# Kernel tuning notes

Measured on AMD Instinct MI355X. Metric: run time of the kernel, lower is better.

The kernel has to match this reference:

```python
import jax, jax.numpy as jnp
import numpy as np

B, L, D, H = 4, 1024, 768, 12
DH = D // H  # 64


def setup_inputs() -> dict:
    key = jax.random.key(0)
    kx, kk, kq, kv = jax.random.split(key, 4)
    # Original uses torch.rand (uniform [0,1)); scale by 1/D so pre-softmax
    # logits stay in a numerically sane range (same math, better conditioning).
    scale = 1.0 / D
    x = jax.random.normal(kx, (B, L, D), dtype=jnp.float32)
    k = jax.random.uniform(kk, (H, D, D), dtype=jnp.float32) * scale
    q = jax.random.uniform(kq, (H, D, D), dtype=jnp.float32) * scale
    v = jax.random.uniform(kv, (H, DH, D), dtype=jnp.float32) * scale
    return {"x": x, "k": k, "q": q, "v": v}


def reference(x, k, q, v):
    # x: [B, L, D]; torch permutes to [B, D, L] then 'bdl,ncd->bncl';
    # equivalent directly: 'bld,ncd->bncl'.
    K = jnp.einsum('bld,ncd->bncl', x, k)   # [B, H, D, L]
    Q = jnp.einsum('bld,ncd->bncl', x, q)   # [B, H, D, L]
    V = jnp.einsum('bld,ncd->bncl', x, v)   # [B, H, DH, L]
    scores = jnp.einsum('bndl,bndm->bnlm', Q, K)        # [B, H, L, L]
    S = jax.nn.softmax(scores, axis=-1)                  # softmax over dim 3
    R = jnp.einsum('bnkl,bndl->bndk', S, V)              # [B, H, DH, L]
    R = R.reshape(x.shape[0], D, -1)                     # [B, D, L]
    return jnp.transpose(R, (0, 2, 1))                   # [B, L, D]
```

## Files before the change

kernel.cpp:

```cpp
#include <hip/hip_runtime.h>
#include <hip/hip_bf16.h>
#include <stdint.h>
#include <stddef.h>

typedef unsigned short u16;
typedef __attribute__((ext_vector_type(8))) short short8;
typedef __attribute__((ext_vector_type(4))) float f32x4;

#define NB 4
#define NL 1024
#define ND 768
#define NH 12
#define NDH 64

__device__ __forceinline__ u16 f2bf(float f) {
  __hip_bfloat16 h = __float2bfloat16(f);
  return *reinterpret_cast<u16*>(&h);
}
__device__ __forceinline__ float bf2f(u16 u) {
  __hip_bfloat16 h;
  *reinterpret_cast<u16*>(&h) = u;
  return __bfloat162float(h);
}

__device__ __forceinline__ void load16_to_lds(const u16* g, u16* l) {
  __builtin_amdgcn_global_load_lds(
      (__attribute__((address_space(1))) void*)(uintptr_t)g,
      (__attribute__((address_space(3))) void*)(uint32_t)(uintptr_t)l,
      16, 0, 0);
}

__global__ __launch_bounds__(256) void cast_bf16_kernel(const float* __restrict__ in,
                                                        u16* __restrict__ out, int n4) {
  int i = blockIdx.x * 256 + threadIdx.x;
  int stride = gridDim.x * 256;
  for (; i < n4; i += stride) {
    float4 f = ((const float4*)in)[i];
    ushort4 o;
    o.x = f2bf(f.x); o.y = f2bf(f.y); o.z = f2bf(f.z); o.w = f2bf(f.w);
    ((ushort4*)out)[i] = o;
  }
}

__global__ __launch_bounds__(256) void transpose_cast_kernel(const float* __restrict__ in,
                                                             u16* __restrict__ out) {
  __shared__ float tile[32][33];
  int h = blockIdx.z;
  const float* src = in + (size_t)h * ND * ND;
  u16* dst = out + (size_t)h * ND * ND;
  int c0 = blockIdx.x * 32, r0 = blockIdx.y * 32;
  int tx = threadIdx.x & 31, ty = threadIdx.x >> 5;
#pragma unroll
  for (int i = 0; i < 32; i += 8)
    tile[ty + i][tx] = src[(size_t)(r0 + ty + i) * ND + c0 + tx];
  __syncthreads();
#pragma unroll
  for (int i = 0; i < 32; i += 8)
    dst[(size_t)(c0 + ty + i) * ND + r0 + tx] = f2bf(tile[tx][ty + i]);
}

template <bool BF16_OUT, int IT, int JT, int KDIM, int LDC, int BK>
__global__ __launch_bounds__(256) void gemm_bt(
    const u16* __restrict__ A, const u16* __restrict__ Bm, void* __restrict__ Cv,
    long sAb, long sAn, long sAz,
    long sBb, long sBn, long sBz,
    long sCb, long sCn, long sCz,
    int p0) {
  constexpr int MTILE = IT * 32;
  constexpr int NTILE = JT * 32;
  constexpr int CPR = BK / 8;
  constexpr int ACH = MTILE * CPR / 256;
  constexpr int BCH = NTILE * CPR / 256;
  constexpr int KC = BK / 32;
  __shared__ __align__(16) u16 As[MTILE * BK];
  __shared__ __align__(16) u16 Bs[NTILE * BK];

  int id = blockIdx.x + gridDim.x * (blockIdx.y + gridDim.y * blockIdx.z);
  int total = gridDim.x * gridDim.y * gridDim.z;
  int xx, yy, zz;
  if ((total & 7) == 0) {
    int per = total >> 3;
    int wk = (id & 7) * per + (id >> 3);
    xx = wk % gridDim.x;
    int g2 = wk / gridDim.x;
    yy = g2 % gridDim.y;
    zz = g2 / gridDim.y;
  } else {
    xx = blockIdx.x; yy = blockIdx.y; zz = blockIdx.z;
  }

  int g = p0 + zz;
  int b = g / NH, n = g % NH;
  A  += (size_t)b * sAb + (size_t)n * sAn + (size_t)zz * sAz;
  Bm += (size_t)b * sBb + (size_t)n * sBn + (size_t)zz * sBz;
  size_t cOff = (size_t)b * sCb + (size_t)n * sCn + (size_t)zz * sCz;

  int m0 = yy * MTILE, n0 = xx * NTILE;
  int t = threadIdx.x;
  int lane = t & 63, w = t >> 6;
  int row16 = lane & 15, q = lane >> 4;
  int wm = w >> 1, wn = w & 1;
  int rsw = (BK == 32) ? ((row16 >> 1) & 3) : (row16 & 7);

  const u16* gA[ACH];
  const u16* gB[BCH];
#pragma unroll
  for (int u = 0; u < ACH; u++) {
    int c = u * 256 + t;
    int r = c / CPR;
    int sw = (BK == 32) ? ((r >> 1) & 3) : (r & 7);
    int cc = (c & (CPR - 1)) ^ sw;
    gA[u] = A + (size_t)(m0 + r) * KDIM + cc * 8;
  }
#pragma unroll
  for (int u = 0; u < BCH; u++) {
    int c = u * 256 + t;
    int r = c / CPR;
    int sw = (BK == 32) ? ((r >> 1) & 3) : (r & 7);
    int cc = (c & (CPR - 1)) ^ sw;
    gB[u] = Bm + (size_t)(n0 + r) * KDIM + cc * 8;
  }

  f32x4 acc[IT][JT];
#pragma unroll
  for (int i = 0; i < IT; i++)
#pragma unroll
    for (int j = 0; j < JT; j++) acc[i][j] = (f32x4){0.f, 0.f, 0.f, 0.f};

#pragma unroll 1
  for (int k0 = 0; k0 < KDIM; k0 += BK) {
    __syncthreads();
#pragma unroll
    for (int u = 0; u < ACH; u++) {
      load16_to_lds(gA[u], &As[(size_t)(u * 256 + w * 64) * 8]);
      gA[u] += BK;
    }
#pragma unroll
    for (int u = 0; u < BCH; u++) {
      load16_to_lds(gB[u], &Bs[(size_t)(u * 256 + w * 64) * 8]);
      gB[u] += BK;
    }
    __syncthreads();

#pragma unroll
    for (int kc = 0; kc < KC; kc++) {
      int ch = ((kc * 4 + q) ^ rsw) * 8;
      short8 af[IT], bfr[JT];
#pragma unroll
      for (int i = 0; i < IT; i++)
        af[i] = *(const short8*)&As[(wm * (IT * 16) + i * 16 + row16) * BK + ch];
#pragma unroll
      for (int j = 0; j < JT; j++)
        bfr[j] = *(const short8*)&Bs[(wn * (JT * 16) + j * 16 + row16) * BK + ch];
#pragma unroll
      for (int i = 0; i < IT; i++)
#pragma unroll
        for (int j = 0; j < JT; j++)
          acc[i][j] = __builtin_amdgcn_mfma_f32_16x16x32_bf16(af[i], bfr[j], acc[i][j], 0, 0, 0);
    }
  }

#pragma unroll
  for (int i = 0; i < IT; i++) {
    int row = m0 + wm * (IT * 16) + i * 16 + q * 4;
#pragma unroll
    for (int j = 0; j < JT; j++) {
      int col = n0 + wn * (JT * 16) + j * 16 + row16;
#pragma unroll
      for (int r = 0; r < 4; r++) {
        float vv = acc[i][j][r];
        if (BF16_OUT) {
          ((u16*)Cv)[cOff + (size_t)(row + r) * LDC + col] = f2bf(vv);
        } else {
          ((float*)Cv)[cOff + (size_t)(row + r) * LDC + col] = vv;
        }
      }
    }
  }
}

__global__ __launch_bounds__(256) void softmax_pv_kernel(
    const u16* __restrict__ Sb, const u16* __restrict__ V2, float* __restrict__ out,
    int p0) {
  __shared__ __align__(16) u16 Ps[128 * 128];
  __shared__ __align__(16) u16 Vs[64 * 128];

  int id = blockIdx.x + gridDim.x * blockIdx.y;
  int total = gridDim.x * gridDim.y;
  int xx, zz;
  if ((total & 7) == 0) {
    int per = total >> 3;
    int wk = (id & 7) * per + (id >> 3);
    xx = wk & 7; zz = wk >> 3;
  } else {
    xx = blockIdx.x; zz = blockIdx.y;
  }

  int g = p0 + zz;
  int b = g / NH, n = g % NH;
  const u16* S = Sb + (size_t)zz * NL * NL;
  const u16* V = V2 + (size_t)zz * NDH * NL;

  int l0 = xx * 128;
  int t = threadIdx.x;
  int lane = t & 63, w = t >> 6;
  int row16 = lane & 15, q = lane >> 4;
  int rs = row16 & 7;

  f32x4 acc[2][5];
#pragma unroll
  for (int i = 0; i < 2; i++)
#pragma unroll
    for (int j = 0; j < 5; j++) acc[i][j] = (f32x4){0.f, 0.f, 0.f, 0.f};

  short8 onesf;
  {
    short val = (row16 == 0) ? (short)0x3F80 : (short)0;
#pragma unroll
    for (int e = 0; e < 8; e++) onesf[e] = val;
  }

#pragma unroll 1
  for (int mt = 0; mt < 8; mt++) {
    int mo = mt * 128;
    __syncthreads();
#pragma unroll
    for (int u = 0; u < 8; u++) {
      int c = u * 256 + t;
      int r = c >> 4, cc = (c & 15) ^ (r & 7);
      load16_to_lds(S + (size_t)(l0 + r) * NL + mo + cc * 8,
                    &Ps[(size_t)(u * 256 + w * 64) * 8]);
    }
#pragma unroll
    for (int u = 0; u < 4; u++) {
      int c = u * 256 + t;
      int r = c >> 4, cc = (c & 15) ^ (r & 7);
      load16_to_lds(V + (size_t)r * NL + mo + cc * 8,
                    &Vs[(size_t)(u * 256 + w * 64) * 8]);
    }
    __syncthreads();

#pragma unroll
    for (int kk = 0; kk < 4; kk++) {
      int ch = ((kk * 4 + q) ^ rs) * 16;
      short8 af[2], bfr[4];
#pragma unroll
      for (int i = 0; i < 2; i++) {
        int row = w * 32 + i * 16 + row16;
        short8 raw = *(const short8*)((const char*)Ps + row * 256 + ch);
        short8 pe;
#pragma unroll
        for (int e = 0; e < 8; e++) pe[e] = (short)f2bf(__expf(bf2f((u16)raw[e])));
        af[i] = pe;
      }
#pragma unroll
      for (int j = 0; j < 4; j++) {
        int row = j * 16 + row16;
        bfr[j] = *(const short8*)((const char*)Vs + row * 256 + ch);
      }
#pragma unroll
      for (int i = 0; i < 2; i++) {
#pragma unroll
        for (int j = 0; j < 4; j++)
          acc[i][j] = __builtin_amdgcn_mfma_f32_16x16x32_bf16(af[i], bfr[j], acc[i][j], 0, 0, 0);
        acc[i][4] = __builtin_amdgcn_mfma_f32_16x16x32_bf16(af[i], onesf, acc[i][4], 0, 0, 0);
      }
    }
  }

#pragma unroll
  for (int i = 0; i < 2; i++) {
#pragma unroll
    for (int r = 0; r < 4; r++) {
      float sum = __shfl(acc[i][4][r], lane & 48, 64);
      float inv = 1.0f / sum;
      int row = l0 + w * 32 + i * 16 + q * 4 + r;
      float* op = out + ((size_t)b * NL + row) * ND + n * NDH;
#pragma unroll
      for (int j = 0; j < 4; j++)
        op[j * 16 + row16] = acc[i][j][r] * inv;
    }
  }
}

extern "C" void kernel_launch(void* const* d_in, const int* in_sizes, int n_in,
                              void* d_out, int out_size, void* d_ws, size_t ws_size,
                              hipStream_t stream) {
  (void)in_sizes; (void)n_in; (void)out_size;
  const float* x  = (const float*)d_in[0];
  const float* kI = (const float*)d_in[1];
  const float* qI = (const float*)d_in[2];
  const float* vI = (const float*)d_in[3];
  float* out = (float*)d_out;

  size_t off = 0;
  char* wsb = (char*)d_ws;
  auto alloc = [&](size_t bytes) -> char* {
    char* p = wsb + off;
    off += (bytes + 255) & ~(size_t)255;
    return p;
  };
  u16* xb = (u16*)alloc((size_t)NB * NL * ND * 2);
  u16* qT = (u16*)alloc((size_t)NH * ND * ND * 2);
  u16* kT = (u16*)alloc((size_t)NH * ND * ND * 2);
  u16* vb = (u16*)alloc((size_t)NH * NDH * ND * 2);
  u16* MT = (u16*)alloc((size_t)NH * ND * ND * 2);
  size_t fixedSz = off;
  const size_t perPair = (size_t)NL * ND * 2 + (size_t)NL * NL * 2 + (size_t)NDH * NL * 2;
  int chunk = NB * NH;
  if (fixedSz + (size_t)chunk * perPair > ws_size) {
    size_t avail = ws_size > fixedSz ? ws_size - fixedSz : 0;
    chunk = (int)(avail / perPair);
    if (chunk < 1) chunk = 1;
    if (chunk > NB * NH) chunk = NB * NH;
  }
  u16* T  = (u16*)alloc((size_t)chunk * NL * ND * 2);
  u16* Sb = (u16*)alloc((size_t)chunk * NL * NL * 2);
  u16* V2 = (u16*)alloc((size_t)chunk * NDH * NL * 2);

  const long DD  = (long)ND * ND;
  const long LD  = (long)NL * ND;
  const long LL  = (long)NL * NL;
  const long DHD = (long)NDH * ND;
  const long DHL = (long)NDH * NL;

  {
    int n4 = NB * NL * ND / 4;
    cast_bf16_kernel<<<dim3((n4 + 255) / 256), dim3(256), 0, stream>>>(x, xb, n4);
    int n4v = NH * NDH * ND / 4;
    cast_bf16_kernel<<<dim3((n4v + 255) / 256), dim3(256), 0, stream>>>(vI, vb, n4v);
  }
  transpose_cast_kernel<<<dim3(24, 24, NH), dim3(256), 0, stream>>>(qI, qT);
  transpose_cast_kernel<<<dim3(24, 24, NH), dim3(256), 0, stream>>>(kI, kT);

  gemm_bt<true, 4, 4, 768, ND, 64><<<dim3(6, 6, NH), dim3(256), 0, stream>>>(
      kT, qT, MT,
      0, DD, 0,  0, DD, 0,  0, DD, 0, 0);

  for (int p0 = 0; p0 < NB * NH; p0 += chunk) {
    int c = NB * NH - p0;
    if (c > chunk) c = chunk;
    gemm_bt<true, 2, 2, 768, NL, 64><<<dim3(16, 1, c), dim3(256), 0, stream>>>(
        vb, xb, V2,
        0, DHD, 0,  LD, 0, 0,  0, 0, DHL, p0);
    gemm_bt<true, 4, 4, 768, ND, 64><<<dim3(6, 8, c), dim3(256), 0, stream>>>(
        xb, MT, T,
        LD, 0, 0,  0, DD, 0,  0, 0, LD, p0);
    gemm_bt<true, 4, 4, 768, NL, 64><<<dim3(8, 8, c), dim3(256), 0, stream>>>(
        T, xb, Sb,
        0, 0, LD,  LD, 0, 0,  0, 0, LL, p0);
    softmax_pv_kernel<<<dim3(8, c), dim3(256), 0, stream>>>(Sb, V2, out, p0);
  }
}
```

Before: 348.7 us.

## Fuse score GEMM into softmax-PV kernel, keeping T tile resident in LDS

Replaces the separate T·xbᵀ score GEMM plus softmax_pv kernel with one fused kernel. Each block holds a 64-row slice of T (64x768 bf16) in LDS, computes 64x128 score tiles against streamed x tiles, exponentiates them into LDS and accumulates P·V together with row sums. This removes the write and re-read of the B*H*L*L bf16 score buffer and one launch. In exchange it uses 144KB of dynamic LDS per block (one block per CU), syncs twice per K step, and runs with fewer blocks (16 per pair) and no multi-stage pipelining.

```diff
diff --git a/kernel.cpp b/kernel.cpp
--- a/kernel.cpp
+++ b/kernel.cpp
@@ -29,6 +29,10 @@
       (__attribute__((address_space(3))) void*)(uint32_t)(uintptr_t)l,
       16, 0, 0);
 }
+
+__device__ __forceinline__ int swz8(int c, int r) { return (c ^ r) & 7; }
+__device__ __forceinline__ int swz16(int c, int r) { return (c & 8) | ((c ^ r) & 7); }
+__device__ __forceinline__ int swzT(int c, int r) { return (c & ~7) | ((c ^ r) & 7); }
 
 __global__ __launch_bounds__(256) void cast_bf16_kernel(const float* __restrict__ in,
                                                         u16* __restrict__ out, int n4) {
@@ -179,39 +183,58 @@
   }
 }
 
-__global__ __launch_bounds__(256) void softmax_pv_kernel(
-    const u16* __restrict__ Sb, const u16* __restrict__ V2, float* __restrict__ out,
-    int p0) {
-  __shared__ __align__(16) u16 Ps[128 * 128];
-  __shared__ __align__(16) u16 Vs[64 * 128];
+__global__ __launch_bounds__(256) void attn_pv_kernel(
+    const u16* __restrict__ T, const u16* __restrict__ xb, const u16* __restrict__ V2,
+    float* __restrict__ out, int p0) {
+  extern __shared__ u16 smem[];
+  u16* Ts = smem;
+  u16* Bs = smem + 49152;
+  u16* Vs = smem + 57344;
+  u16* Ss = smem + 65536;
 
   int id = blockIdx.x + gridDim.x * blockIdx.y;
-  int total = gridDim.x * gridDim.y;
-  int xx, zz;
-  if ((total & 7) == 0) {
-    int per = total >> 3;
-    int wk = (id & 7) * per + (id >> 3);
-    xx = wk & 7; zz = wk >> 3;
-  } else {
-    xx = blockIdx.x; zz = blockIdx.y;
-  }
+  int per = (gridDim.x * gridDim.y) >> 3;
+  int wk = (id & 7) * per + (id >> 3);
+  int xx = wk & 15, zz = wk >> 4;
 
   int g = p0 + zz;
   int b = g / NH, n = g % NH;
-  const u16* S = Sb + (size_t)zz * NL * NL;
-  const u16* V = V2 + (size_t)zz * NDH * NL;
-
-  int l0 = xx * 128;
+  const u16* Tz = T + (size_t)zz * NL * ND + (size_t)xx * 64 * ND;
+  const u16* xbb = xb + (size_t)b * NL * ND;
+  const u16* Vz = V2 + (size_t)zz * NDH * NL;
+  int l0 = xx * 64;
+
   int t = threadIdx.x;
   int lane = t & 63, w = t >> 6;
   int row16 = lane & 15, q = lane >> 4;
-  int rs = row16 & 7;
-
-  f32x4 acc[2][5];
-#pragma unroll
-  for (int i = 0; i < 2; i++)
-#pragma unroll
-    for (int j = 0; j < 5; j++) acc[i][j] = (f32x4){0.f, 0.f, 0.f, 0.f};
+  int wm = w >> 1, wn = w & 1;
+
+#pragma unroll
+  for (int u = 0; u < 24; u++) {
+    int c = u * 256 + t;
+    int r = c / 96, rem = c - r * 96;
+    int lg = swzT(rem, r);
+    load16_to_lds(Tz + (size_t)r * ND + lg * 8, &Ts[(size_t)(u * 256 + w * 64) * 8]);
+  }
+
+  const u16* bsrc[4];
+#pragma unroll
+  for (int u = 0; u < 4; u++) {
+    int c = u * 256 + t;
+    int r = c >> 3, cc = (c & 7) ^ (r & 7);
+    bsrc[u] = xbb + (size_t)r * ND + cc * 8;
+  }
+  const u16* vsrc[4];
+#pragma unroll
+  for (int u = 0; u < 4; u++) {
+    int c = u * 256 + t;
+    int r = c >> 4, cc = (c & 15) ^ (r & 7);
+    vsrc[u] = Vz + (size_t)r * NL + cc * 8;
+  }
+
+  f32x4 acc_o[5];
+#pragma unroll
+  for (int j = 0; j < 5; j++) acc_o[j] = (f32x4){0.f, 0.f, 0.f, 0.f};
 
   short8 onesf;
   {
@@ -225,61 +248,85 @@
     int mo = mt * 128;
     __syncthreads();
 #pragma unroll
-    for (int u = 0; u < 8; u++) {
-      int c = u * 256 + t;
-      int r = c >> 4, cc = (c & 15) ^ (r & 7);
-      load16_to_lds(S + (size_t)(l0 + r) * NL + mo + cc * 8,
-                    &Ps[(size_t)(u * 256 + w * 64) * 8]);
-    }
-#pragma unroll
-    for (int u = 0; u < 4; u++) {
-      int c = u * 256 + t;
-      int r = c >> 4, cc = (c & 15) ^ (r & 7);
-      load16_to_lds(V + (size_t)r * NL + mo + cc * 8,
-                    &Vs[(size_t)(u * 256 + w * 64) * 8]);
+    for (int u = 0; u < 4; u++)
+      load16_to_lds(vsrc[u] + mo, &Vs[(size_t)(u * 256 + w * 64) * 8]);
+
+    f32x4 acc_s[2][4];
+#pragma unroll
+    for (int i = 0; i < 2; i++)
+#pragma unroll
+      for (int j = 0; j < 4; j++) acc_s[i][j] = (f32x4){0.f, 0.f, 0.f, 0.f};
+
+#pragma unroll 1
+    for (int kb = 0; kb < 12; kb++) {
+      __syncthreads();
+#pragma unroll
+      for (int u = 0; u < 4; u++)
+        load16_to_lds(bsrc[u] + ((size_t)mo * ND + kb * 64), &Bs[(size_t)(u * 256 + w * 64) * 8]);
+      __syncthreads();
+
+#pragma unroll
+      for (int kc = 0; kc < 2; kc++) {
+        short8 af[2], bfr[4];
+#pragma unroll
+        for (int i = 0; i < 2; i++) {
+          int l = wm * 32 + i * 16 + row16;
+          int ck = kb * 8 + kc * 4 + q;
+          af[i] = *(const short8*)&Ts[l * ND + swzT(ck, l) * 8];
+        }
+#pragma unroll
+        for (int j = 0; j < 4; j++) {
+          int r = wn * 64 + j * 16 + row16;
+          bfr[j] = *(const short8*)&Bs[r * 64 + swz8(kc * 4 + q, r) * 8];
+        }
+#pragma unroll
+        for (int i = 0; i < 2; i++)
+#pragma unroll
+          for (int j = 0; j < 4; j++)
+            acc_s[i][j] = __builtin_amdgcn_mfma_f32_16x16x32_bf16(af[i], bfr[j], acc_s[i][j], 0, 0, 0);
+      }
+    }
+
+#pragma unroll
+    for (int i = 0; i < 2; i++) {
+#pragma unroll
+      for (int j = 0; j < 4; j++) {
+#pragma unroll
+        for (int r = 0; r < 4; r++) {
+          int l = wm * 32 + i * 16 + q * 4 + r;
+          int col = wn * 64 + j * 16 + row16;
+          Ss[l * 128 + swz16(col >> 3, l) * 8 + (col & 7)] = f2bf(__expf(acc_s[i][j][r]));
+        }
+      }
     }
     __syncthreads();
 
 #pragma unroll
     for (int kk = 0; kk < 4; kk++) {
-      int ch = ((kk * 4 + q) ^ rs) * 16;
-      short8 af[2], bfr[4];
-#pragma unroll
-      for (int i = 0; i < 2; i++) {
-        int row = w * 32 + i * 16 + row16;
-        short8 raw = *(const short8*)((const char*)Ps + row * 256 + ch);
-        short8 pe;
-#pragma unroll
-        for (int e = 0; e < 8; e++) pe[e] = (short)f2bf(__expf(bf2f((u16)raw[e])));
-        af[i] = pe;
+      int l = w * 16 + row16;
+      short8 af = *(const short8*)&Ss[l * 128 + swz16(kk * 4 + q, l) * 8];
+      short8 bfr[4];
+#pragma unroll
+      for (int j = 0; j < 4; j++) {
+        int dh = j * 16 + row16;
+        bfr[j] = *(const short8*)&Vs[dh * 128 + swz16(kk * 4 + q, dh) * 8];
       }
 #pragma unroll
-      for (int j = 0; j < 4; j++) {
-        int row = j * 16 + row16;
-        bfr[j] = *(const short8*)((const char*)Vs + row * 256 + ch);
-      }
-#pragma unroll
-      for (int i = 0; i < 2; i++) {
-#pragma unroll
-        for (int j = 0; j < 4; j++)
-          acc[i][j] = __builtin_amdgcn_mfma_f32_16x16x32_bf16(af[i], bfr[j], acc[i][j], 0, 0, 0);
-        acc[i][4] = __builtin_amdgcn_mfma_f32_16x16x32_bf16(af[i], onesf, acc[i][4], 0, 0, 0);
-      }
-    }
-  }
-
-#pragma unroll
-  for (int i = 0; i < 2; i++) {
-#pragma unroll
-    for (int r = 0; r < 4; r++) {
-      float sum = __shfl(acc[i][4][r], lane & 48, 64);
-      float inv = 1.0f / sum;
-      int row = l0 + w * 32 + i * 16 + q * 4 + r;
-      float* op = out + ((size_t)b * NL + row) * ND + n * NDH;
-#pragma unroll
       for (int j = 0; j < 4; j++)
-        op[j * 16 + row16] = acc[i][j][r] * inv;
-    }
+        acc_o[j] = __builtin_amdgcn_mfma_f32_16x16x32_bf16(af, bfr[j], acc_o[j], 0, 0, 0);
+      acc_o[4] = __builtin_amdgcn_mfma_f32_16x16x32_bf16(af, onesf, acc_o[4], 0, 0, 0);
+    }
+  }
+
+#pragma unroll
+  for (int r = 0; r < 4; r++) {
+    float sum = __shfl(acc_o[4][r], lane & 48, 64);
+    float inv = 1.0f / sum;
+    int row = l0 + w * 16 + q * 4 + r;
+    float* op = out + ((size_t)b * NL + row) * ND + n * NDH;
+#pragma unroll
+    for (int j = 0; j < 4; j++)
+      op[j * 16 + row16] = acc_o[j][r] * inv;
   }
 }
 
@@ -306,7 +353,7 @@
   u16* vb = (u16*)alloc((size_t)NH * NDH * ND * 2);
   u16* MT = (u16*)alloc((size_t)NH * ND * ND * 2);
   size_t fixedSz = off;
-  const size_t perPair = (size_t)NL * ND * 2 + (size_t)NL * NL * 2 + (size_t)NDH * NL * 2;
+  const size_t perPair = (size_t)NL * ND * 2 + (size_t)NDH * NL * 2;
   int chunk = NB * NH;
   if (fixedSz + (size_t)chunk * perPair > ws_size) {
     size_t avail = ws_size > fixedSz ? ws_size - fixedSz : 0;
@@ -315,14 +362,15 @@
     if (chunk > NB * NH) chunk = NB * NH;
   }
   u16* T  = (u16*)alloc((size_t)chunk * NL * ND * 2);
-  u16* Sb = (u16*)alloc((size_t)chunk * NL * NL * 2);
   u16* V2 = (u16*)alloc((size_t)chunk * NDH * NL * 2);
 
   const long DD  = (long)ND * ND;
   const long LD  = (long)NL * ND;
-  const long LL  = (long)NL * NL;
   const long DHD = (long)NDH * ND;
   const long DHL = (long)NDH * NL;
+
+  hipFuncSetAttribute((const void*)attn_pv_kernel,
+                      hipFuncAttributeMaxDynamicSharedMemorySize, 147456);
 
   {
     int n4 = NB * NL * ND / 4;
@@ -346,9 +394,6 @@
     gemm_bt<true, 4, 4, 768, ND, 64><<<dim3(6, 8, c), dim3(256), 0, stream>>>(
         xb, MT, T,
         LD, 0, 0,  0, DD, 0,  0, 0, LD, p0);
-    gemm_bt<true, 4, 4, 768, NL, 64><<<dim3(8, 8, c), dim3(256), 0, stream>>>(
-        T, xb, Sb,
-        0, 0, LD,  LD, 0, 0,  0, 0, LL, p0);
-    softmax_pv_kernel<<<dim3(8, c), dim3(256), 0, stream>>>(Sb, V2, out, p0);
-  }
-}
+    attn_pv_kernel<<<dim3(16, c), dim3(256), 147456, stream>>>(T, xb, V2, out, p0);
+  }
+}
```

After: 501.3 us. +43.8%, slower.

## Switch GEMMs to 32x32x16 MFMA and halve softmax-PV row tile

Applied to the files above, without the earlier changes.

The generic bt-GEMM now computes each wave's output with 32x32x16 bf16 MFMA instructions and 16-float accumulators instead of 16x16x32. Tile sizes stay the same (IM*64 equals the old IT*32) and the K step is fixed at 64. The larger instruction should cut LDS fragment reads and instruction count per FLOP. Separately, the softmax-PV kernel processes 64 query rows per block instead of 128 and launches twice as many blocks, with the global source pointers hoisted out of the loop. This trades more V reloads for more parallelism and lower LDS use.

```diff
diff --git a/kernel.cpp b/kernel.cpp
--- a/kernel.cpp
+++ b/kernel.cpp
@@ -6,6 +6,7 @@
 typedef unsigned short u16;
 typedef __attribute__((ext_vector_type(8))) short short8;
 typedef __attribute__((ext_vector_type(4))) float f32x4;
+typedef __attribute__((ext_vector_type(16))) float f32x16;
 
 #define NB 4
 #define NL 1024
@@ -59,19 +60,19 @@
     dst[(size_t)(c0 + ty + i) * ND + r0 + tx] = f2bf(tile[tx][ty + i]);
 }
 
-template <bool BF16_OUT, int IT, int JT, int KDIM, int LDC, int BK>
+template <bool BF16_OUT, int IM, int IN, int KDIM, int LDC>
 __global__ __launch_bounds__(256) void gemm_bt(
     const u16* __restrict__ A, const u16* __restrict__ Bm, void* __restrict__ Cv,
     long sAb, long sAn, long sAz,
     long sBb, long sBn, long sBz,
     long sCb, long sCn, long sCz,
     int p0) {
-  constexpr int MTILE = IT * 32;
-  constexpr int NTILE = JT * 32;
+  constexpr int BK = 64;
+  constexpr int MTILE = IM * 64;
+  constexpr int NTILE = IN * 64;
   constexpr int CPR = BK / 8;
   constexpr int ACH = MTILE * CPR / 256;
   constexpr int BCH = NTILE * CPR / 256;
-  constexpr int KC = BK / 32;
   __shared__ __align__(16) u16 As[MTILE * BK];
   __shared__ __align__(16) u16 Bs[NTILE * BK];
 
@@ -98,9 +99,8 @@
   int m0 = yy * MTILE, n0 = xx * NTILE;
   int t = threadIdx.x;
   int lane = t & 63, w = t >> 6;
-  int row16 = lane & 15, q = lane >> 4;
+  int m32 = lane & 31, kg = lane >> 5;
   int wm = w >> 1, wn = w & 1;
-  int rsw = (BK == 32) ? ((row16 >> 1) & 3) : (row16 & 7);
 
   const u16* gA[ACH];
   const u16* gB[BCH];
@@ -108,24 +108,24 @@
   for (int u = 0; u < ACH; u++) {
     int c = u * 256 + t;
     int r = c / CPR;
-    int sw = (BK == 32) ? ((r >> 1) & 3) : (r & 7);
-    int cc = (c & (CPR - 1)) ^ sw;
+    int cc = (c & (CPR - 1)) ^ (r & 7);
     gA[u] = A + (size_t)(m0 + r) * KDIM + cc * 8;
   }
 #pragma unroll
   for (int u = 0; u < BCH; u++) {
     int c = u * 256 + t;
     int r = c / CPR;
-    int sw = (BK == 32) ? ((r >> 1) & 3) : (r & 7);
-    int cc = (c & (CPR - 1)) ^ sw;
+    int cc = (c & (CPR - 1)) ^ (r & 7);
     gB[u] = Bm + (size_t)(n0 + r) * KDIM + cc * 8;
   }
 
-  f32x4 acc[IT][JT];
-#pragma unroll
-  for (int i = 0; i < IT; i++)
-#pragma unroll
-    for (int j = 0; j < JT; j++) acc[i][j] = (f32x4){0.f, 0.f, 0.f, 0.f};
+  f32x16 acc[IM][IN];
+#pragma unroll
+  for (int i = 0; i < IM; i++)
+#pragma unroll
+    for (int j = 0; j < IN; j++)
+#pragma unroll
+      for (int r = 0; r < 16; r++) acc[i][j][r] = 0.f;
 
 #pragma unroll 1
   for (int k0 = 0; k0 < KDIM; k0 += BK) {
@@ -143,36 +143,49 @@
     __syncthreads();
 
 #pragma unroll
-    for (int kc = 0; kc < KC; kc++) {
-      int ch = ((kc * 4 + q) ^ rsw) * 8;
-      short8 af[IT], bfr[JT];
-#pragma unroll
-      for (int i = 0; i < IT; i++)
-        af[i] = *(const short8*)&As[(wm * (IT * 16) + i * 16 + row16) * BK + ch];
-#pragma unroll
-      for (int j = 0; j < JT; j++)
-        bfr[j] = *(const short8*)&Bs[(wn * (JT * 16) + j * 16 + row16) * BK + ch];
-#pragma unroll
-      for (int i = 0; i < IT; i++)
-#pragma unroll
-        for (int j = 0; j < JT; j++)
-          acc[i][j] = __builtin_amdgcn_mfma_f32_16x16x32_bf16(af[i], bfr[j], acc[i][j], 0, 0, 0);
-    }
-  }
-
-#pragma unroll
-  for (int i = 0; i < IT; i++) {
-    int row = m0 + wm * (IT * 16) + i * 16 + q * 4;
-#pragma unroll
-    for (int j = 0; j < JT; j++) {
-      int col = n0 + wn * (JT * 16) + j * 16 + row16;
-#pragma unroll
-      for (int r = 0; r < 4; r++) {
+    for (int kc = 0; kc < 2; kc++) {
+      short8 af[IM][2], bfr[IN][2];
+#pragma unroll
+      for (int i = 0; i < IM; i++) {
+        int row = wm * (IM * 32) + i * 32 + m32;
+#pragma unroll
+        for (int h = 0; h < 2; h++) {
+          int ck = (kc * 4 + h * 2 + kg) ^ (row & 7);
+          af[i][h] = *(const short8*)&As[row * BK + ck * 8];
+        }
+      }
+#pragma unroll
+      for (int j = 0; j < IN; j++) {
+        int row = wn * (IN * 32) + j * 32 + m32;
+#pragma unroll
+        for (int h = 0; h < 2; h++) {
+          int ck = (kc * 4 + h * 2 + kg) ^ (row & 7);
+          bfr[j][h] = *(const short8*)&Bs[row * BK + ck * 8];
+        }
+      }
+#pragma unroll
+      for (int i = 0; i < IM; i++)
+#pragma unroll
+        for (int j = 0; j < IN; j++) {
+          acc[i][j] = __builtin_amdgcn_mfma_f32_32x32x16_bf16(af[i][0], bfr[j][0], acc[i][j], 0, 0, 0);
+          acc[i][j] = __builtin_amdgcn_mfma_f32_32x32x16_bf16(af[i][1], bfr[j][1], acc[i][j], 0, 0, 0);
+        }
+    }
+  }
+
+#pragma unroll
+  for (int i = 0; i < IM; i++) {
+#pragma unroll
+    for (int j = 0; j < IN; j++) {
+      int colg = n0 + wn * (IN * 32) + j * 32 + m32;
+#pragma unroll
+      for (int r = 0; r < 16; r++) {
+        int rowg = m0 + wm * (IM * 32) + i * 32 + (r & 3) + 8 * (r >> 2) + 4 * kg;
         float vv = acc[i][j][r];
         if (BF16_OUT) {
-          ((u16*)Cv)[cOff + (size_t)(row + r) * LDC + col] = f2bf(vv);
+          ((u16*)Cv)[cOff + (size_t)rowg * LDC + colg] = f2bf(vv);
         } else {
-          ((float*)Cv)[cOff + (size_t)(row + r) * LDC + col] = vv;
+          ((float*)Cv)[cOff + (size_t)rowg * LDC + colg] = vv;
         }
       }
     }
@@ -182,7 +195,7 @@
 __global__ __launch_bounds__(256) void softmax_pv_kernel(
     const u16* __restrict__ Sb, const u16* __restrict__ V2, float* __restrict__ out,
     int p0) {
-  __shared__ __align__(16) u16 Ps[128 * 128];
+  __shared__ __align__(16) u16 Ps[64 * 128];
   __shared__ __align__(16) u16 Vs[64 * 128];
 
   int id = blockIdx.x + gridDim.x * blockIdx.y;
@@ -191,7 +204,7 @@
   if ((total & 7) == 0) {
     int per = total >> 3;
     int wk = (id & 7) * per + (id >> 3);
-    xx = wk & 7; zz = wk >> 3;
+    xx = wk & 15; zz = wk >> 4;
   } else {
     xx = blockIdx.x; zz = blockIdx.y;
   }
@@ -201,23 +214,31 @@
   const u16* S = Sb + (size_t)zz * NL * NL;
   const u16* V = V2 + (size_t)zz * NDH * NL;
 
-  int l0 = xx * 128;
+  int l0 = xx * 64;
   int t = threadIdx.x;
   int lane = t & 63, w = t >> 6;
   int row16 = lane & 15, q = lane >> 4;
   int rs = row16 & 7;
 
-  f32x4 acc[2][5];
-#pragma unroll
-  for (int i = 0; i < 2; i++)
-#pragma unroll
-    for (int j = 0; j < 5; j++) acc[i][j] = (f32x4){0.f, 0.f, 0.f, 0.f};
+  f32x4 acc[5];
+#pragma unroll
+  for (int j = 0; j < 5; j++) acc[j] = (f32x4){0.f, 0.f, 0.f, 0.f};
 
   short8 onesf;
   {
     short val = (row16 == 0) ? (short)0x3F80 : (short)0;
 #pragma unroll
     for (int e = 0; e < 8; e++) onesf[e] = val;
+  }
+
+  const u16* ssrc[4];
+  const u16* vsrc[4];
+#pragma unroll
+  for (int u = 0; u < 4; u++) {
+    int c = u * 256 + t;
+    int r = c >> 4, cc = (c & 15) ^ (r & 7);
+    ssrc[u] = S + (size_t)(l0 + r) * NL + cc * 8;
+    vsrc[u] = V + (size_t)r * NL + cc * 8;
   }
 
 #pragma unroll 1
@@ -225,61 +246,43 @@
     int mo = mt * 128;
     __syncthreads();
 #pragma unroll
-    for (int u = 0; u < 8; u++) {
-      int c = u * 256 + t;
-      int r = c >> 4, cc = (c & 15) ^ (r & 7);
-      load16_to_lds(S + (size_t)(l0 + r) * NL + mo + cc * 8,
-                    &Ps[(size_t)(u * 256 + w * 64) * 8]);
-    }
-#pragma unroll
-    for (int u = 0; u < 4; u++) {
-      int c = u * 256 + t;
-      int r = c >> 4, cc = (c & 15) ^ (r & 7);
-      load16_to_lds(V + (size_t)r * NL + mo + cc * 8,
-                    &Vs[(size_t)(u * 256 + w * 64) * 8]);
-    }
+    for (int u = 0; u < 4; u++)
+      load16_to_lds(ssrc[u] + mo, &Ps[(size_t)(u * 256 + w * 64) * 8]);
+#pragma unroll
+    for (int u = 0; u < 4; u++)
+      load16_to_lds(vsrc[u] + mo, &Vs[(size_t)(u * 256 + w * 64) * 8]);
     __syncthreads();
 
 #pragma unroll
     for (int kk = 0; kk < 4; kk++) {
       int ch = ((kk * 4 + q) ^ rs) * 16;
-      short8 af[2], bfr[4];
-#pragma unroll
-      for (int i = 0; i < 2; i++) {
-        int row = w * 32 + i * 16 + row16;
-        short8 raw = *(const short8*)((const char*)Ps + row * 256 + ch);
-        short8 pe;
-#pragma unroll
-        for (int e = 0; e < 8; e++) pe[e] = (short)f2bf(__expf(bf2f((u16)raw[e])));
-        af[i] = pe;
+      int lrow = w * 16 + row16;
+      short8 raw = *(const short8*)((const char*)Ps + lrow * 256 + ch);
+      short8 af;
+#pragma unroll
+      for (int e = 0; e < 8; e++) af[e] = (short)f2bf(__expf(bf2f((u16)raw[e])));
+      short8 bfr[4];
+#pragma unroll
+      for (int j = 0; j < 4; j++) {
+        int dh = j * 16 + row16;
+        bfr[j] = *(const short8*)((const char*)Vs + dh * 256 + ch);
       }
 #pragma unroll
-      for (int j = 0; j < 4; j++) {
-        int row = j * 16 + row16;
-        bfr[j] = *(const short8*)((const char*)Vs + row * 256 + ch);
-      }
-#pragma unroll
-      for (int i = 0; i < 2; i++) {
-#pragma unroll
-        for (int j = 0; j < 4; j++)
-          acc[i][j] = __builtin_amdgcn_mfma_f32_16x16x32_bf16(af[i], bfr[j], acc[i][j], 0, 0, 0);
-        acc[i][4] = __builtin_amdgcn_mfma_f32_16x16x32_bf16(af[i], onesf, acc[i][4], 0, 0, 0);
-      }
-    }
-  }
-
-#pragma unroll
-  for (int i = 0; i < 2; i++) {
-#pragma unroll
-    for (int r = 0; r < 4; r++) {
-      float sum = __shfl(acc[i][4][r], lane & 48, 64);
-      float inv = 1.0f / sum;
-      int row = l0 + w * 32 + i * 16 + q * 4 + r;
-      float* op = out + ((size_t)b * NL + row) * ND + n * NDH;
-#pragma unroll
       for (int j = 0; j < 4; j++)
-        op[j * 16 + row16] = acc[i][j][r] * inv;
-    }
+        acc[j] = __builtin_amdgcn_mfma_f32_16x16x32_bf16(af, bfr[j], acc[j], 0, 0, 0);
+      acc[4] = __builtin_amdgcn_mfma_f32_16x16x32_bf16(af, onesf, acc[4], 0, 0, 0);
+    }
+  }
+
+#pragma unroll
+  for (int r = 0; r < 4; r++) {
+    float sum = __shfl(acc[4][r], lane & 48, 64);
+    float inv = 1.0f / sum;
+    int row = l0 + w * 16 + q * 4 + r;
+    float* op = out + ((size_t)b * NL + row) * ND + n * NDH;
+#pragma unroll
+    for (int j = 0; j < 4; j++)
+      op[j * 16 + row16] = acc[j][r] * inv;
   }
 }
 
@@ -333,22 +336,22 @@
   transpose_cast_kernel<<<dim3(24, 24, NH), dim3(256), 0, stream>>>(qI, qT);
   transpose_cast_kernel<<<dim3(24, 24, NH), dim3(256), 0, stream>>>(kI, kT);
 
-  gemm_bt<true, 4, 4, 768, ND, 64><<<dim3(6, 6, NH), dim3(256), 0, stream>>>(
+  gemm_bt<true, 2, 2, 768, ND><<<dim3(6, 6, NH), dim3(256), 0, stream>>>(
       kT, qT, MT,
       0, DD, 0,  0, DD, 0,  0, DD, 0, 0);
 
   for (int p0 = 0; p0 < NB * NH; p0 += chunk) {
     int c = NB * NH - p0;
     if (c > chunk) c = chunk;
-    gemm_bt<true, 2, 2, 768, NL, 64><<<dim3(16, 1, c), dim3(256), 0, stream>>>(
+    gemm_bt<true, 1, 1, 768, NL><<<dim3(16, 1, c), dim3(256), 0, stream>>>(
         vb, xb, V2,
         0, DHD, 0,  LD, 0, 0,  0, 0, DHL, p0);
-    gemm_bt<true, 4, 4, 768, ND, 64><<<dim3(6, 8, c), dim3(256), 0, stream>>>(
+    gemm_bt<true, 2, 2, 768, ND><<<dim3(6, 8, c), dim3(256), 0, stream>>>(
         xb, MT, T,
         LD, 0, 0,  0, DD, 0,  0, 0, LD, p0);
-    gemm_bt<true, 4, 4, 768, NL, 64><<<dim3(8, 8, c), dim3(256), 0, stream>>>(
+    gemm_bt<true, 2, 2, 768, NL><<<dim3(8, 8, c), dim3(256), 0, stream>>>(
         T, xb, Sb,
         0, 0, LD,  LD, 0, 0,  0, 0, LL, p0);
-    softmax_pv_kernel<<<dim3(8, c), dim3(256), 0, stream>>>(Sb, V2, out, p0);
-  }
-}
+    softmax_pv_kernel<<<dim3(16, c), dim3(256), 0, stream>>>(Sb, V2, out, p0);
+  }
+}
```

Result: faster. 318.6 us (-8.6%).
